# Performance work log

Hardware: AMD Instinct MI355X
Metric: run time of the kernel (lower is better)

## Reference

```python
import jax, jax.numpy as jnp
import numpy as np
from jax import lax

EPS = 1e-5
B = 512

def _conv(x, w, pad):
    # x: [B,Cin,H,W], w: [Cout,Cin,kh,kw]
    return lax.conv_general_dilated(x, w, (1, 1), [(pad, pad), (pad, pad)],
                                    dimension_numbers=('NCHW', 'OIHW', 'NCHW'))

def _bn2d(x, g, b, m, v):
    s = g * lax.rsqrt(v + EPS)
    return x * s[None, :, None, None] + (b - m * s)[None, :, None, None]

def _bn1d(x, g, b, m, v):
    s = g * lax.rsqrt(v + EPS)
    return x * s + (b - m * s)

def _pool2(x):
    return lax.reduce_window(x, -jnp.inf, lax.max, (1, 1, 2, 2), (1, 1, 2, 2), 'VALID')

def setup_inputs() -> dict:
    key = jax.random.key(0)
    ks = iter(jax.random.split(key, 64))
    rn = lambda shape, s=1.0: jax.random.normal(next(ks), shape, dtype=jnp.float32) * s
    un = lambda shape: jax.random.uniform(next(ks), shape, dtype=jnp.float32, minval=0.5, maxval=1.5)
    def bn_params(c):
        return (jnp.ones((c,), jnp.float32), jnp.zeros((c,), jnp.float32), rn((c,), 0.1), un((c,)))
    inp = {"x": rn((B, 3, 64, 64))}
    inp["w1"] = rn((32, 3, 5, 5), 0.1)
    inp["bn1_g"], inp["bn1_b"], inp["bn1_m"], inp["bn1_v"] = bn_params(32)
    inp["w2"] = rn((64, 32, 3, 3), 0.06)
    inp["bn2_g"], inp["bn2_b"], inp["bn2_m"], inp["bn2_v"] = bn_params(64)
    inp["w3"] = rn((128, 64, 3, 3), 0.04)
    inp["bn3_g"], inp["bn3_b"], inp["bn3_m"], inp["bn3_v"] = bn_params(128)
    inp["fc_w"] = rn((256, 8192), 0.01)
    inp["fc_b"] = jnp.zeros((256,), jnp.float32)
    inp["bnf_g"], inp["bnf_b"], inp["bnf_m"], inp["bnf_v"] = bn_params(256)
    inp["c_w1"] = rn((64, 256), 0.06)
    inp["c_b1"] = jnp.zeros((64,), jnp.float32)
    inp["bnc_g"], inp["bnc_b"], inp["bnc_m"], inp["bnc_v"] = bn_params(64)
    inp["c_w2"] = rn((1, 64), 0.1)
    inp["c_b2"] = jnp.zeros((1,), jnp.float32)
    inp["m_w1"] = rn((64, 256), 0.06)
    inp["m_b1"] = jnp.zeros((64,), jnp.float32)
    inp["bnm_g"], inp["bnm_b"], inp["bnm_m"], inp["bnm_v"] = bn_params(64)
    inp["m_w2"] = rn((1, 64), 0.1)
    inp["m_b2"] = jnp.zeros((1,), jnp.float32)
    return inp

def reference(x, w1, bn1_g, bn1_b, bn1_m, bn1_v,
              w2, bn2_g, bn2_b, bn2_m, bn2_v,
              w3, bn3_g, bn3_b, bn3_m, bn3_v,
              fc_w, fc_b, bnf_g, bnf_b, bnf_m, bnf_v,
              c_w1, c_b1, bnc_g, bnc_b, bnc_m, bnc_v, c_w2, c_b2,
              m_w1, m_b1, bnm_g, bnm_b, bnm_m, bnm_v, m_w2, m_b2):
    # Block 1: conv5x5(3->32) + BN + ReLU + maxpool2 -> [B,32,32,32]
    h = _pool2(jax.nn.relu(_bn2d(_conv(x, w1, 2), bn1_g, bn1_b, bn1_m, bn1_v)))
    # Block 2: conv3x3(32->64) + BN + ReLU + maxpool2 -> [B,64,16,16]
    h = _pool2(jax.nn.relu(_bn2d(_conv(h, w2, 1), bn2_g, bn2_b, bn2_m, bn2_v)))
    # Block 3: conv3x3(64->128) + BN + ReLU + maxpool2 + ToDense -> [B,128,8,8]
    h = _pool2(jax.nn.relu(_bn2d(_conv(h, w3, 1), bn3_g, bn3_b, bn3_m, bn3_v)))
    f = h.reshape(h.shape[0], -1)  # [B, 8192]
    s = jax.nn.relu(_bn1d(f @ fc_w.T + fc_b, bnf_g, bnf_b, bnf_m, bnf_v))  # [B,256]
    c = jax.nn.relu(_bn1d(s @ c_w1.T + c_b1, bnc_g, bnc_b, bnc_m, bnc_v)) @ c_w2.T + c_b2
    mo = jax.nn.relu(_bn1d(s @ m_w1.T + m_b1, bnm_g, bnm_b, bnm_m, bnm_v)) @ m_w2.T + m_b2
    return (c, mo)  # ([B,1], [B,1])
```

## Files before the change

kernel.cpp:

```cpp
#include <hip/hip_runtime.h>
#include <hip/hip_bf16.h>

#define EPS 1e-5f

typedef __attribute__((ext_vector_type(8))) short bf16x8;
typedef __attribute__((ext_vector_type(4))) float f32x4;

__device__ __forceinline__ ushort f2b(float f) {
    return __builtin_bit_cast(ushort, __float2bfloat16(f));
}
__device__ __forceinline__ bf16x8 ld_frag(const char* p) {
    return __builtin_bit_cast(bf16x8, *reinterpret_cast<const uint4*>(p));
}

__global__ __launch_bounds__(256) void k_prep(
    const float* __restrict__ w1, const float* __restrict__ w2,
    const float* __restrict__ w3,
    ushort* __restrict__ w1p, ushort* __restrict__ w2p, ushort* __restrict__ w3p)
{
    const int total = 5120 + 18432 + 73728;
    for (int i = blockIdx.x * 256 + threadIdx.x; i < total; i += gridDim.x * 256) {
        if (i < 5120) {
            const int ky = i >> 10, co = (i >> 5) & 31, k = i & 31;
            const int kx = k >> 2, ci = k & 3;
            float v = 0.f;
            if (kx < 5 && ci < 3) v = w1[((co * 3 + ci) * 5 + ky) * 5 + kx];
            w1p[i] = f2b(v);
        } else if (i < 5120 + 18432) {
            const int j = i - 5120;
            const int tap = j >> 11, co = (j >> 5) & 63, ci = j & 31;
            w2p[j] = f2b(w2[(co * 32 + ci) * 9 + tap]);
        } else {
            const int j = i - (5120 + 18432);
            const int tap = j >> 13, co = (j >> 6) & 127, ci = j & 63;
            w3p[j] = f2b(w3[(co * 64 + ci) * 9 + tap]);
        }
    }
}

__global__ __launch_bounds__(256) void k_prep_fc(
    const float* __restrict__ fcw, ushort* __restrict__ fcwp)
{
    __shared__ ushort l[128 * 66];
    const int j = blockIdx.x, t = threadIdx.x;
    const float* src = fcw + (size_t)j * 8192;
    #pragma unroll
    for (int i = 0; i < 32; ++i) {
        const int idx = i * 256 + t;
        const int c = idx >> 6, p = idx & 63;
        l[c * 66 + p] = f2b(src[idx]);
    }
    __syncthreads();
    ushort* dst = fcwp + (size_t)j * 8192;
    #pragma unroll
    for (int i = 0; i < 32; ++i) {
        const int idx = i * 256 + t;
        const int c = idx & 127, p = idx >> 7;
        dst[idx] = l[c * 66 + p];
    }
}

__global__ __launch_bounds__(256) void k_conv1(
    const float* __restrict__ x, const ushort* __restrict__ w1p,
    const float* __restrict__ bg, const float* __restrict__ bb,
    const float* __restrict__ bm, const float* __restrict__ bv,
    ushort* __restrict__ h1)
{
    __shared__ __align__(16) ushort xs[12 * 72 * 4];
    __shared__ __align__(16) ushort ws[5 * 32 * 32];
    const int bid = blockIdx.x;
    const int n = bid >> 3, q = bid & 7;
    const int t = threadIdx.x;
    const int wave = t >> 6, lane = t & 63;
    const int g = lane >> 4, l15 = lane & 15;

    for (int idx = t; idx < 864; idx += 256) {
        const int row = idx / 72, col = idx - row * 72;
        const int gr = 8 * q - 2 + row, gc = col - 2;
        ushort p0 = 0, p1 = 0, p2 = 0;
        if ((unsigned)gr < 64u && (unsigned)gc < 64u) {
            const size_t base = ((size_t)n * 3 << 12) + (gr << 6) + gc;
            p0 = f2b(x[base]); p1 = f2b(x[base + 4096]); p2 = f2b(x[base + 8192]);
        }
        ushort4 pk; pk.x = p0; pk.y = p1; pk.z = p2; pk.w = 0;
        *reinterpret_cast<ushort4*>(&xs[idx * 4]) = pk;
    }
    for (int i = t; i < 640; i += 256) {
        const int gg = i & 3, r = i >> 2;
        const int co = r & 31;
        const uint4 v = *reinterpret_cast<const uint4*>(&w1p[r * 32 + gg * 8]);
        *reinterpret_cast<uint4*>((char*)ws + r * 64 + ((gg ^ ((co >> 1) & 3)) << 4)) = v;
    }
    __syncthreads();

    f32x4 acc[8][2];
    #pragma unroll
    for (int i = 0; i < 8; ++i) { acc[i][0] = (f32x4){0,0,0,0}; acc[i][1] = (f32x4){0,0,0,0}; }

    const char* xsb = (const char*)xs;
    const char* wsb = (const char*)ws;
    #pragma unroll
    for (int ky = 0; ky < 5; ++ky) {
        bf16x8 a[8], b[2];
        #pragma unroll
        for (int mt = 0; mt < 8; ++mt) {
            const int crl = 2 * wave + (mt >> 2);
            const int ccl = (mt & 3) * 16 + l15;
            const int off = ((crl + ky) * 72 + ccl) * 8 + g * 16;
            const uint2 lo = *reinterpret_cast<const uint2*>(xsb + off);
            const uint2 hi = *reinterpret_cast<const uint2*>(xsb + off + 8);
            uint4 all; all.x = lo.x; all.y = lo.y; all.z = hi.x; all.w = hi.y;
            a[mt] = __builtin_bit_cast(bf16x8, all);
        }
        #pragma unroll
        for (int nt = 0; nt < 2; ++nt) {
            const int co = nt * 16 + l15;
            b[nt] = ld_frag(wsb + (ky * 32 + co) * 64 + ((g ^ ((co >> 1) & 3)) << 4));
        }
        #pragma unroll
        for (int mt = 0; mt < 8; ++mt)
            #pragma unroll
            for (int nt = 0; nt < 2; ++nt)
                acc[mt][nt] = __builtin_amdgcn_mfma_f32_16x16x32_bf16(a[mt], b[nt], acc[mt][nt], 0, 0, 0);
    }

    const int prow = q * 4 + wave;
    #pragma unroll
    for (int nt = 0; nt < 2; ++nt) {
        const int co = nt * 16 + l15;
        const float s = bg[co] * rsqrtf(bv[co] + EPS);
        const float bsv = bb[co] - bm[co] * s;
        #pragma unroll
        for (int mt = 0; mt < 4; ++mt) {
            #pragma unroll
            for (int j = 0; j < 2; ++j) {
                const float v0 = fmaxf(fmaf(acc[mt][nt][2 * j],     s, bsv), 0.f);
                const float v1 = fmaxf(fmaf(acc[mt][nt][2 * j + 1], s, bsv), 0.f);
                const float v2 = fmaxf(fmaf(acc[mt + 4][nt][2 * j],     s, bsv), 0.f);
                const float v3 = fmaxf(fmaf(acc[mt + 4][nt][2 * j + 1], s, bsv), 0.f);
                const int ppc = mt * 8 + g * 2 + j;
                h1[(((size_t)n * 32 + prow) * 32 + ppc) * 32 + co] =
                    f2b(fmaxf(fmaxf(v0, v1), fmaxf(v2, v3)));
            }
        }
    }
}

__global__ __launch_bounds__(256) void k_conv2(
    const ushort* __restrict__ h1, const ushort* __restrict__ w2p,
    const float* __restrict__ bg, const float* __restrict__ bb,
    const float* __restrict__ bm, const float* __restrict__ bv,
    ushort* __restrict__ h2)
{
    __shared__ __align__(16) ushort xs[10 * 34 * 32];
    __shared__ __align__(16) ushort ws[9 * 64 * 32];
    const int bid = blockIdx.x;
    const int n = bid >> 2, q = bid & 3;
    const int t = threadIdx.x;
    const int wave = t >> 6, lane = t & 63;
    const int g = lane >> 4, l15 = lane & 15;

    for (int i = t; i < 1360; i += 256) {
        const int gg = i & 3, pix = i >> 2;
        const int row = pix / 34, col = pix - row * 34;
        const int gr = 8 * q - 1 + row, gc = col - 1;
        uint4 v = {0, 0, 0, 0};
        if ((unsigned)gr < 32u && (unsigned)gc < 32u)
            v = *reinterpret_cast<const uint4*>(&h1[((((size_t)n * 32 + gr) * 32 + gc) << 5) + gg * 8]);
        *reinterpret_cast<uint4*>((char*)xs + pix * 64 + ((gg ^ ((pix >> 1) & 3)) << 4)) = v;
    }
    for (int i = t; i < 2304; i += 256) {
        const int gg = i & 3, r = i >> 2;
        const int co = r & 63;
        const uint4 v = *reinterpret_cast<const uint4*>(&w2p[r * 32 + gg * 8]);
        *reinterpret_cast<uint4*>((char*)ws + r * 64 + ((gg ^ ((co >> 1) & 3)) << 4)) = v;
    }
    __syncthreads();

    f32x4 acc[4][4];
    #pragma unroll
    for (int i = 0; i < 4; ++i)
        #pragma unroll
        for (int j = 0; j < 4; ++j) acc[i][j] = (f32x4){0,0,0,0};

    const char* xsb = (const char*)xs;
    const char* wsb = (const char*)ws;
    #pragma unroll
    for (int tap = 0; tap < 9; ++tap) {
        const int ky = tap / 3, kx = tap - 3 * ky;
        bf16x8 a[4], b[4];
        #pragma unroll
        for (int mt = 0; mt < 4; ++mt) {
            const int crl = 2 * wave + (mt >> 1);
            const int ccl = (mt & 1) * 16 + l15;
            const int pix = (crl + ky) * 34 + ccl + kx;
            a[mt] = ld_frag(xsb + pix * 64 + ((g ^ ((pix >> 1) & 3)) << 4));
        }
        #pragma unroll
        for (int nt = 0; nt < 4; ++nt) {
            const int co = nt * 16 + l15;
            b[nt] = ld_frag(wsb + (tap * 64 + co) * 64 + ((g ^ ((co >> 1) & 3)) << 4));
        }
        #pragma unroll
        for (int mt = 0; mt < 4; ++mt)
            #pragma unroll
            for (int nt = 0; nt < 4; ++nt)
                acc[mt][nt] = __builtin_amdgcn_mfma_f32_16x16x32_bf16(a[mt], b[nt], acc[mt][nt], 0, 0, 0);
    }
    __syncthreads();

    const int prow = q * 4 + wave;
    #pragma unroll
    for (int nt = 0; nt < 4; ++nt) {
        const int co = nt * 16 + l15;
        const float s = bg[co] * rsqrtf(bv[co] + EPS);
        const float bsv = bb[co] - bm[co] * s;
        #pragma unroll
        for (int mtl = 0; mtl < 2; ++mtl) {
            #pragma unroll
            for (int j = 0; j < 2; ++j) {
                const float v0 = fmaxf(fmaf(acc[mtl][nt][2 * j],     s, bsv), 0.f);
                const float v1 = fmaxf(fmaf(acc[mtl][nt][2 * j + 1], s, bsv), 0.f);
                const float v2 = fmaxf(fmaf(acc[mtl + 2][nt][2 * j],     s, bsv), 0.f);
                const float v3 = fmaxf(fmaf(acc[mtl + 2][nt][2 * j + 1], s, bsv), 0.f);
                const int ppc = mtl * 8 + g * 2 + j;
                h2[(((size_t)n * 16 + prow) * 16 + ppc) * 64 + co] =
                    f2b(fmaxf(fmaxf(v0, v1), fmaxf(v2, v3)));
            }
        }
    }
}

__global__ __launch_bounds__(256) void k_conv3(
    const ushort* __restrict__ h2, const ushort* __restrict__ w3p,
    const float* __restrict__ bg, const float* __restrict__ bb,
    const float* __restrict__ bm, const float* __restrict__ bv,
    ushort* __restrict__ h3)
{
    __shared__ __align__(16) ushort xs[18 * 18 * 32];
    __shared__ __align__(16) ushort ws[9 * 64 * 32];
    const int bid = blockIdx.x;
    const int n = bid >> 1, ch = bid & 1;
    const int t = threadIdx.x;
    const int wave = t >> 6, lane = t & 63;
    const int g = lane >> 4, l15 = lane & 15;

    f32x4 acc[4][4];
    #pragma unroll
    for (int i = 0; i < 4; ++i)
        #pragma unroll
        for (int j = 0; j < 4; ++j) acc[i][j] = (f32x4){0,0,0,0};

    const char* xsb = (const char*)xs;
    const char* wsb = (const char*)ws;

    for (int gci = 0; gci < 2; ++gci) {
        if (gci) __syncthreads();
        for (int i = t; i < 1296; i += 256) {
            const int gg = i & 3, pix = i >> 2;
            const int row = pix / 18, col = pix - row * 18;
            const int gr = row - 1, gc = col - 1;
            uint4 v = {0, 0, 0, 0};
            if ((unsigned)gr < 16u && (unsigned)gc < 16u)
                v = *reinterpret_cast<const uint4*>(
                    &h2[((((size_t)n * 16 + gr) * 16 + gc) << 6) + gci * 32 + gg * 8]);
            *reinterpret_cast<uint4*>((char*)xs + pix * 64 + ((gg ^ ((pix >> 1) & 3)) << 4)) = v;
        }
        for (int i = t; i < 2304; i += 256) {
            const int gg = i & 3, r = i >> 2;
            const int tap = r >> 6, co = r & 63;
            const uint4 v = *reinterpret_cast<const uint4*>(
                &w3p[((size_t)(tap * 128 + ch * 64 + co) << 6) + gci * 32 + gg * 8]);
            *reinterpret_cast<uint4*>((char*)ws + r * 64 + ((gg ^ ((co >> 1) & 3)) << 4)) = v;
        }
        __syncthreads();
        #pragma unroll
        for (int tap = 0; tap < 9; ++tap) {
            const int ky = tap / 3, kx = tap - 3 * ky;
            bf16x8 a[4], b[4];
            #pragma unroll
            for (int mt = 0; mt < 4; ++mt) {
                const int pr = 4 * wave + mt;
                const int pix = (pr + ky) * 18 + l15 + kx;
                a[mt] = ld_frag(xsb + pix * 64 + ((g ^ ((pix >> 1) & 3)) << 4));
            }
            #pragma unroll
            for (int nt = 0; nt < 4; ++nt) {
                const int co = nt * 16 + l15;
                b[nt] = ld_frag(wsb + (tap * 64 + co) * 64 + ((g ^ ((co >> 1) & 3)) << 4));
            }
            #pragma unroll
            for (int mt = 0; mt < 4; ++mt)
                #pragma unroll
                for (int nt = 0; nt < 4; ++nt)
                    acc[mt][nt] = __builtin_amdgcn_mfma_f32_16x16x32_bf16(a[mt], b[nt], acc[mt][nt], 0, 0, 0);
        }
    }

    #pragma unroll
    for (int nt = 0; nt < 4; ++nt) {
        const int co = ch * 64 + nt * 16 + l15;
        const float s = bg[co] * rsqrtf(bv[co] + EPS);
        const float bsv = bb[co] - bm[co] * s;
        #pragma unroll
        for (int mtl = 0; mtl < 2; ++mtl) {
            #pragma unroll
            for (int j = 0; j < 2; ++j) {
                const int mt = mtl * 2;
                const float v0 = fmaxf(fmaf(acc[mt][nt][2 * j],     s, bsv), 0.f);
                const float v1 = fmaxf(fmaf(acc[mt][nt][2 * j + 1], s, bsv), 0.f);
                const float v2 = fmaxf(fmaf(acc[mt + 1][nt][2 * j],     s, bsv), 0.f);
                const float v3 = fmaxf(fmaf(acc[mt + 1][nt][2 * j + 1], s, bsv), 0.f);
                const int ppr = 2 * wave + mtl;
                const int ppc = g * 2 + j;
                h3[(((size_t)n * 8 + ppr) * 8 + ppc) * 128 + co] =
                    f2b(fmaxf(fmaxf(v0, v1), fmaxf(v2, v3)));
            }
        }
    }
}

__global__ __launch_bounds__(256) void k_fc(
    const ushort* __restrict__ A, const ushort* __restrict__ Bw, float* __restrict__ C)
{
    __shared__ __align__(16) ushort As[64 * 32];
    __shared__ __align__(16) ushort Bs[64 * 32];
    const int bm = blockIdx.x, bn = blockIdx.y, kz = blockIdx.z;
    const int t = threadIdx.x;
    const int wave = t >> 6, lane = t & 63;
    const int g = lane >> 4, l15 = lane & 15;

    f32x4 acc[4];
    #pragma unroll
    for (int i = 0; i < 4; ++i) acc[i] = (f32x4){0,0,0,0};

    const char* asb = (const char*)As;
    const char* bsb = (const char*)Bs;
    for (int kk = 0; kk < 16; ++kk) {
        const int k0 = kz * 512 + kk * 32;
        if (kk) __syncthreads();
        {
            const int gg = t & 3, row = t >> 2;
            const uint4 va = *reinterpret_cast<const uint4*>(
                &A[(size_t)(bm * 64 + row) * 8192 + k0 + gg * 8]);
            *reinterpret_cast<uint4*>((char*)As + row * 64 + ((gg ^ ((row >> 1) & 3)) << 4)) = va;
            const uint4 vb = *reinterpret_cast<const uint4*>(
                &Bw[(size_t)(bn * 64 + row) * 8192 + k0 + gg * 8]);
            *reinterpret_cast<uint4*>((char*)Bs + row * 64 + ((gg ^ ((row >> 1) & 3)) << 4)) = vb;
        }
        __syncthreads();
        bf16x8 a[4], b;
        #pragma unroll
        for (int mt = 0; mt < 4; ++mt) {
            const int r = mt * 16 + l15;
            a[mt] = ld_frag(asb + r * 64 + ((g ^ ((r >> 1) & 3)) << 4));
        }
        {
            const int r = wave * 16 + l15;
            b = ld_frag(bsb + r * 64 + ((g ^ ((r >> 1) & 3)) << 4));
        }
        #pragma unroll
        for (int mt = 0; mt < 4; ++mt)
            acc[mt] = __builtin_amdgcn_mfma_f32_16x16x32_bf16(a[mt], b, acc[mt], 0, 0, 0);
    }

    float* Cp = C + (size_t)kz * 512 * 256;
    const int col = bn * 64 + wave * 16 + l15;
    #pragma unroll
    for (int mt = 0; mt < 4; ++mt) {
        #pragma unroll
        for (int r = 0; r < 4; ++r) {
            const int row = bm * 64 + mt * 16 + g * 4 + r;
            Cp[(size_t)row * 256 + col] = acc[mt][r];
        }
    }
}

__global__ __launch_bounds__(128) void k_heads(
    const float* __restrict__ sraw, const float* __restrict__ fcb,
    const float* __restrict__ fg, const float* __restrict__ fb,
    const float* __restrict__ fm, const float* __restrict__ fv,
    const float* __restrict__ cw1, const float* __restrict__ cb1,
    const float* __restrict__ cg, const float* __restrict__ cbb,
    const float* __restrict__ cm, const float* __restrict__ cv,
    const float* __restrict__ cw2, const float* __restrict__ cb2,
    const float* __restrict__ mw1, const float* __restrict__ mb1,
    const float* __restrict__ mg, const float* __restrict__ mbb,
    const float* __restrict__ mm, const float* __restrict__ mv,
    const float* __restrict__ mw2, const float* __restrict__ mb2,
    float* __restrict__ outp)
{
    __shared__ float sv[256];
    const int b = blockIdx.x, t = threadIdx.x;
    for (int k = t; k < 256; k += 128) {
        float val = fcb[k];
        #pragma unroll
        for (int z = 0; z < 16; ++z) val += sraw[(size_t)z * 131072 + b * 256 + k];
        const float s = fg[k] * rsqrtf(fv[k] + EPS);
        sv[k] = fmaxf(fmaf(val, s, fb[k] - fm[k] * s), 0.f);
    }
    __syncthreads();
    const int j = t & 63;
    const bool isM = (t >= 64);
    const float* w1  = isM ? mw1 : cw1;
    const float* b1  = isM ? mb1 : cb1;
    const float* g1  = isM ? mg  : cg;
    const float* bb1 = isM ? mbb : cbb;
    const float* m1  = isM ? mm  : cm;
    const float* v1  = isM ? mv  : cv;
    const float* w2  = isM ? mw2 : cw2;
    const float* b2  = isM ? mb2 : cb2;
    float d = 0.f;
    const float* wr = w1 + j * 256;
    #pragma unroll 8
    for (int k = 0; k < 256; ++k) d = fmaf(sv[k], wr[k], d);
    d += b1[j];
    const float s1 = g1[j] * rsqrtf(v1[j] + EPS);
    d = fmaxf(fmaf(d, s1, bb1[j] - m1[j] * s1), 0.f);
    float prod = d * w2[j];
    #pragma unroll
    for (int off = 32; off > 0; off >>= 1) prod += __shfl_down(prod, off);
    if (j == 0) outp[(isM ? 512 : 0) + b] = prod + b2[0];
}

extern "C" void kernel_launch(void* const* d_in, const int* in_sizes, int n_in,
                              void* d_out, int out_size, void* d_ws, size_t ws_size,
                              hipStream_t stream)
{
    const float* x    = (const float*)d_in[0];
    const float* w1   = (const float*)d_in[1];
    const float* bn1g = (const float*)d_in[2];
    const float* bn1b = (const float*)d_in[3];
    const float* bn1m = (const float*)d_in[4];
    const float* bn1v = (const float*)d_in[5];
    const float* w2   = (const float*)d_in[6];
    const float* bn2g = (const float*)d_in[7];
    const float* bn2b = (const float*)d_in[8];
    const float* bn2m = (const float*)d_in[9];
    const float* bn2v = (const float*)d_in[10];
    const float* w3   = (const float*)d_in[11];
    const float* bn3g = (const float*)d_in[12];
    const float* bn3b = (const float*)d_in[13];
    const float* bn3m = (const float*)d_in[14];
    const float* bn3v = (const float*)d_in[15];
    const float* fcw  = (const float*)d_in[16];
    const float* fcb  = (const float*)d_in[17];
    const float* bnfg = (const float*)d_in[18];
    const float* bnfb = (const float*)d_in[19];
    const float* bnfm = (const float*)d_in[20];
    const float* bnfv = (const float*)d_in[21];
    const float* cw1  = (const float*)d_in[22];
    const float* cb1  = (const float*)d_in[23];
    const float* bncg = (const float*)d_in[24];
    const float* bncb = (const float*)d_in[25];
    const float* bncm = (const float*)d_in[26];
    const float* bncv = (const float*)d_in[27];
    const float* cw2  = (const float*)d_in[28];
    const float* cb2  = (const float*)d_in[29];
    const float* mw1  = (const float*)d_in[30];
    const float* mb1  = (const float*)d_in[31];
    const float* bnmg = (const float*)d_in[32];
    const float* bnmb = (const float*)d_in[33];
    const float* bnmm = (const float*)d_in[34];
    const float* bnmv = (const float*)d_in[35];
    const float* mw2  = (const float*)d_in[36];
    const float* mb2  = (const float*)d_in[37];

    char* W = (char*)d_ws;
    ushort* h1   = (ushort*)(W);
    ushort* h2   = (ushort*)(W + 33554432);
    ushort* h3   = (ushort*)(W + 50331648);
    ushort* w1p  = (ushort*)(W + 58720256);
    ushort* w2p  = (ushort*)(W + 58730496);
    ushort* w3p  = (ushort*)(W + 58767360);
    ushort* fcwp = (ushort*)(W + 58914816);
    float*  sr   = (float*) (W + 63109120);
    float* outp = (float*)d_out;

    k_prep<<<128, 256, 0, stream>>>(w1, w2, w3, w1p, w2p, w3p);
    k_prep_fc<<<256, 256, 0, stream>>>(fcw, fcwp);
    k_conv1<<<512 * 8, 256, 0, stream>>>(x, w1p, bn1g, bn1b, bn1m, bn1v, h1);
    k_conv2<<<512 * 4, 256, 0, stream>>>(h1, w2p, bn2g, bn2b, bn2m, bn2v, h2);
    k_conv3<<<512 * 2, 256, 0, stream>>>(h2, w3p, bn3g, bn3b, bn3m, bn3v, h3);
    k_fc<<<dim3(8, 4, 16), 256, 0, stream>>>(h3, fcwp, sr);
    k_heads<<<512, 128, 0, stream>>>(sr, fcb, bnfg, bnfb, bnfm, bnfv,
                                     cw1, cb1, bncg, bncb, bncm, bncv, cw2, cb2,
                                     mw1, mb1, bnmg, bnmb, bnmm, bnmv, mw2, mb2, outp);
}
```

Measured before the change: 254.4 us.

## Pre-pad activations in global memory, merge prep kernels, and batch images per conv block

All prep work is merged into one kernel. That kernel also converts the input to a zero-padded, 4-channel bf16 layout and zeroes the halo borders of padded h1 and h2 buffers. Conv1 and conv2 then write into these padded buffers, so conv2 and conv3 can load tiles with plain vectorized copies and no bounds checks. Conv2 now loops over 4 images per block, and conv3 has each block handle 2 images with more M tiles per wave, so weights staged in shared memory are reused. The costs are an extra pass over the input, a larger workspace, fewer blocks, and higher register pressure in conv3.

```diff
diff --git a/kernel.cpp b/kernel.cpp
--- a/kernel.cpp
+++ b/kernel.cpp
@@ -13,58 +13,97 @@
     return __builtin_bit_cast(bf16x8, *reinterpret_cast<const uint4*>(p));
 }
 
-__global__ __launch_bounds__(256) void k_prep(
+__global__ __launch_bounds__(256) void k_prep_all(
     const float* __restrict__ w1, const float* __restrict__ w2,
-    const float* __restrict__ w3,
-    ushort* __restrict__ w1p, ushort* __restrict__ w2p, ushort* __restrict__ w3p)
-{
-    const int total = 5120 + 18432 + 73728;
-    for (int i = blockIdx.x * 256 + threadIdx.x; i < total; i += gridDim.x * 256) {
-        if (i < 5120) {
-            const int ky = i >> 10, co = (i >> 5) & 31, k = i & 31;
-            const int kx = k >> 2, ci = k & 3;
-            float v = 0.f;
-            if (kx < 5 && ci < 3) v = w1[((co * 3 + ci) * 5 + ky) * 5 + kx];
-            w1p[i] = f2b(v);
-        } else if (i < 5120 + 18432) {
-            const int j = i - 5120;
-            const int tap = j >> 11, co = (j >> 5) & 63, ci = j & 31;
-            w2p[j] = f2b(w2[(co * 32 + ci) * 9 + tap]);
-        } else {
-            const int j = i - (5120 + 18432);
-            const int tap = j >> 13, co = (j >> 6) & 127, ci = j & 63;
-            w3p[j] = f2b(w3[(co * 64 + ci) * 9 + tap]);
-        }
-    }
-}
-
-__global__ __launch_bounds__(256) void k_prep_fc(
-    const float* __restrict__ fcw, ushort* __restrict__ fcwp)
+    const float* __restrict__ w3, const float* __restrict__ fcw,
+    const float* __restrict__ x,
+    ushort* __restrict__ w1p, ushort* __restrict__ w2p, ushort* __restrict__ w3p,
+    ushort* __restrict__ fcwp, ushort* __restrict__ x4p,
+    ushort* __restrict__ h1p, ushort* __restrict__ h2p)
 {
     __shared__ ushort l[128 * 66];
-    const int j = blockIdx.x, t = threadIdx.x;
-    const float* src = fcw + (size_t)j * 8192;
-    #pragma unroll
-    for (int i = 0; i < 32; ++i) {
-        const int idx = i * 256 + t;
-        const int c = idx >> 6, p = idx & 63;
-        l[c * 66 + p] = f2b(src[idx]);
-    }
-    __syncthreads();
-    ushort* dst = fcwp + (size_t)j * 8192;
-    #pragma unroll
-    for (int i = 0; i < 32; ++i) {
-        const int idx = i * 256 + t;
-        const int c = idx & 127, p = idx >> 7;
-        dst[idx] = l[c * 66 + p];
+    const int bid = blockIdx.x, t = threadIdx.x;
+    if (bid < 128) {
+        const int total = 5120 + 18432 + 73728;
+        for (int i = bid * 256 + t; i < total; i += 128 * 256) {
+            if (i < 5120) {
+                const int ky = i >> 10, co = (i >> 5) & 31, k = i & 31;
+                const int kx = k >> 2, ci = k & 3;
+                float v = 0.f;
+                if (kx < 5 && ci < 3) v = w1[((co * 3 + ci) * 5 + ky) * 5 + kx];
+                w1p[i] = f2b(v);
+            } else if (i < 5120 + 18432) {
+                const int j = i - 5120;
+                const int tap = j >> 11, co = (j >> 5) & 63, ci = j & 31;
+                w2p[j] = f2b(w2[(co * 32 + ci) * 9 + tap]);
+            } else {
+                const int j = i - (5120 + 18432);
+                const int tap = j >> 13, co = (j >> 6) & 127, ci = j & 63;
+                w3p[j] = f2b(w3[(co * 64 + ci) * 9 + tap]);
+            }
+        }
+    } else if (bid < 384) {
+        const int j = bid - 128;
+        const float* src = fcw + (size_t)j * 8192;
+        #pragma unroll
+        for (int i = 0; i < 32; ++i) {
+            const int idx = i * 256 + t;
+            const int c = idx >> 6, p = idx & 63;
+            l[c * 66 + p] = f2b(src[idx]);
+        }
+        __syncthreads();
+        ushort* dst = fcwp + (size_t)j * 8192;
+        #pragma unroll
+        for (int i = 0; i < 32; ++i) {
+            const int idx = i * 256 + t;
+            const int c = idx & 127, p = idx >> 7;
+            dst[idx] = l[c * 66 + p];
+        }
+    } else if (bid < 4480) {
+        for (int p = (bid - 384) * 256 + t; p < 2506752; p += 4096 * 256) {
+            const int n = p / 4896;
+            const int rem = p - n * 4896;
+            const int row = rem / 72, col = rem - row * 72;
+            const int gr = row - 2, gc = col - 2;
+            ushort4 pk; pk.x = 0; pk.y = 0; pk.z = 0; pk.w = 0;
+            if ((unsigned)gr < 64u && (unsigned)gc < 64u) {
+                const size_t base = ((size_t)n * 3 << 12) + (gr << 6) + gc;
+                pk.x = f2b(x[base]); pk.y = f2b(x[base + 4096]); pk.z = f2b(x[base + 8192]);
+            }
+            *reinterpret_cast<ushort4*>(&x4p[(size_t)p * 4]) = pk;
+        }
+    } else if (bid < 4736) {
+        const uint4 z = {0, 0, 0, 0};
+        for (int i = (bid - 4480) * 256 + t; i < 270336; i += 256 * 256) {
+            const int img = i / 528;
+            const int rem = i - img * 528;
+            const int px = rem >> 2, gg = rem & 3;
+            int row, col;
+            if (px < 34)      { row = 0;  col = px; }
+            else if (px < 68) { row = 33; col = px - 34; }
+            else { const int q = px - 68; row = 1 + (q >> 1); col = (q & 1) ? 33 : 0; }
+            *reinterpret_cast<uint4*>(&h1p[(((size_t)img * 34 + row) * 34 + col) * 32 + gg * 8]) = z;
+        }
+    } else if (bid < 4992) {
+        const uint4 z = {0, 0, 0, 0};
+        for (int i = (bid - 4736) * 256 + t; i < 278528; i += 256 * 256) {
+            const int img = i / 544;
+            const int rem = i - img * 544;
+            const int px = rem >> 3, gg = rem & 7;
+            int row, col;
+            if (px < 18)      { row = 0;  col = px; }
+            else if (px < 36) { row = 17; col = px - 18; }
+            else { const int q = px - 36; row = 1 + (q >> 1); col = (q & 1) ? 17 : 0; }
+            *reinterpret_cast<uint4*>(&h2p[(((size_t)img * 18 + row) * 18 + col) * 64 + gg * 8]) = z;
+        }
     }
 }
 
 __global__ __launch_bounds__(256) void k_conv1(
-    const float* __restrict__ x, const ushort* __restrict__ w1p,
+    const ushort* __restrict__ x4p, const ushort* __restrict__ w1p,
     const float* __restrict__ bg, const float* __restrict__ bb,
     const float* __restrict__ bm, const float* __restrict__ bv,
-    ushort* __restrict__ h1)
+    ushort* __restrict__ h1p)
 {
     __shared__ __align__(16) ushort xs[12 * 72 * 4];
     __shared__ __align__(16) ushort ws[5 * 32 * 32];
@@ -74,16 +113,10 @@
     const int wave = t >> 6, lane = t & 63;
     const int g = lane >> 4, l15 = lane & 15;
 
-    for (int idx = t; idx < 864; idx += 256) {
-        const int row = idx / 72, col = idx - row * 72;
-        const int gr = 8 * q - 2 + row, gc = col - 2;
-        ushort p0 = 0, p1 = 0, p2 = 0;
-        if ((unsigned)gr < 64u && (unsigned)gc < 64u) {
-            const size_t base = ((size_t)n * 3 << 12) + (gr << 6) + gc;
-            p0 = f2b(x[base]); p1 = f2b(x[base + 4096]); p2 = f2b(x[base + 8192]);
-        }
-        ushort4 pk; pk.x = p0; pk.y = p1; pk.z = p2; pk.w = 0;
-        *reinterpret_cast<ushort4*>(&xs[idx * 4]) = pk;
+    {
+        const ushort* src = x4p + ((size_t)(n * 68 + 8 * q) * 72) * 4;
+        for (int i = t; i < 432; i += 256)
+            *reinterpret_cast<uint4*>(&xs[i * 8]) = *reinterpret_cast<const uint4*>(src + i * 8);
     }
     for (int i = t; i < 640; i += 256) {
         const int gg = i & 3, r = i >> 2;
@@ -139,132 +172,136 @@
                 const float v2 = fmaxf(fmaf(acc[mt + 4][nt][2 * j],     s, bsv), 0.f);
                 const float v3 = fmaxf(fmaf(acc[mt + 4][nt][2 * j + 1], s, bsv), 0.f);
                 const int ppc = mt * 8 + g * 2 + j;
-                h1[(((size_t)n * 32 + prow) * 32 + ppc) * 32 + co] =
+                h1p[(((size_t)n * 34 + prow + 1) * 34 + ppc + 1) * 32 + co] =
                     f2b(fmaxf(fmaxf(v0, v1), fmaxf(v2, v3)));
             }
         }
     }
 }
 
-__global__ __launch_bounds__(256) void k_conv2(
-    const ushort* __restrict__ h1, const ushort* __restrict__ w2p,
+__global__ __launch_bounds__(256, 2) void k_conv2(
+    const ushort* __restrict__ h1p, const ushort* __restrict__ w2p,
     const float* __restrict__ bg, const float* __restrict__ bb,
     const float* __restrict__ bm, const float* __restrict__ bv,
-    ushort* __restrict__ h2)
+    ushort* __restrict__ h2p)
 {
     __shared__ __align__(16) ushort xs[10 * 34 * 32];
     __shared__ __align__(16) ushort ws[9 * 64 * 32];
     const int bid = blockIdx.x;
-    const int n = bid >> 2, q = bid & 3;
+    const int ngrp = bid >> 2, q = bid & 3;
     const int t = threadIdx.x;
     const int wave = t >> 6, lane = t & 63;
     const int g = lane >> 4, l15 = lane & 15;
-
-    for (int i = t; i < 1360; i += 256) {
-        const int gg = i & 3, pix = i >> 2;
-        const int row = pix / 34, col = pix - row * 34;
-        const int gr = 8 * q - 1 + row, gc = col - 1;
-        uint4 v = {0, 0, 0, 0};
-        if ((unsigned)gr < 32u && (unsigned)gc < 32u)
-            v = *reinterpret_cast<const uint4*>(&h1[((((size_t)n * 32 + gr) * 32 + gc) << 5) + gg * 8]);
-        *reinterpret_cast<uint4*>((char*)xs + pix * 64 + ((gg ^ ((pix >> 1) & 3)) << 4)) = v;
-    }
+    const char* xsb = (const char*)xs;
+    const char* wsb = (const char*)ws;
+
     for (int i = t; i < 2304; i += 256) {
         const int gg = i & 3, r = i >> 2;
         const int co = r & 63;
         const uint4 v = *reinterpret_cast<const uint4*>(&w2p[r * 32 + gg * 8]);
         *reinterpret_cast<uint4*>((char*)ws + r * 64 + ((gg ^ ((co >> 1) & 3)) << 4)) = v;
     }
-    __syncthreads();
-
-    f32x4 acc[4][4];
-    #pragma unroll
-    for (int i = 0; i < 4; ++i)
-        #pragma unroll
-        for (int j = 0; j < 4; ++j) acc[i][j] = (f32x4){0,0,0,0};
-
-    const char* xsb = (const char*)xs;
-    const char* wsb = (const char*)ws;
-    #pragma unroll
-    for (int tap = 0; tap < 9; ++tap) {
-        const int ky = tap / 3, kx = tap - 3 * ky;
-        bf16x8 a[4], b[4];
-        #pragma unroll
-        for (int mt = 0; mt < 4; ++mt) {
-            const int crl = 2 * wave + (mt >> 1);
-            const int ccl = (mt & 1) * 16 + l15;
-            const int pix = (crl + ky) * 34 + ccl + kx;
-            a[mt] = ld_frag(xsb + pix * 64 + ((g ^ ((pix >> 1) & 3)) << 4));
-        }
+
+    for (int img = 0; img < 4; ++img) {
+        const int n = ngrp * 4 + img;
+        if (img) __syncthreads();
+        {
+            const ushort* src = h1p + ((size_t)(n * 34 + 8 * q) * 34) * 32;
+            for (int i = t; i < 1360; i += 256) {
+                const int gg = i & 3, pix = i >> 2;
+                const uint4 v = *reinterpret_cast<const uint4*>(src + i * 8);
+                *reinterpret_cast<uint4*>((char*)xs + pix * 64 + ((gg ^ ((pix >> 1) & 3)) << 4)) = v;
+            }
+        }
+        __syncthreads();
+
+        f32x4 acc[4][4];
+        #pragma unroll
+        for (int i = 0; i < 4; ++i)
+            #pragma unroll
+            for (int j = 0; j < 4; ++j) acc[i][j] = (f32x4){0,0,0,0};
+
+        #pragma unroll
+        for (int tap = 0; tap < 9; ++tap) {
+            const int ky = tap / 3, kx = tap - 3 * ky;
+            bf16x8 a[4], b[4];
+            #pragma unroll
+            for (int mt = 0; mt < 4; ++mt) {
+                const int crl = 2 * wave + (mt >> 1);
+                const int ccl = (mt & 1) * 16 + l15;
+                const int pix = (crl + ky) * 34 + ccl + kx;
+                a[mt] = ld_frag(xsb + pix * 64 + ((g ^ ((pix >> 1) & 3)) << 4));
+            }
+            #pragma unroll
+            for (int nt = 0; nt < 4; ++nt) {
+                const int co = nt * 16 + l15;
+                b[nt] = ld_frag(wsb + (tap * 64 + co) * 64 + ((g ^ ((co >> 1) & 3)) << 4));
+            }
+            #pragma unroll
+            for (int mt = 0; mt < 4; ++mt)
+                #pragma unroll
+                for (int nt = 0; nt < 4; ++nt)
+                    acc[mt][nt] = __builtin_amdgcn_mfma_f32_16x16x32_bf16(a[mt], b[nt], acc[mt][nt], 0, 0, 0);
+        }
+
+        const int prow = q * 4 + wave;
         #pragma unroll
         for (int nt = 0; nt < 4; ++nt) {
             const int co = nt * 16 + l15;
-            b[nt] = ld_frag(wsb + (tap * 64 + co) * 64 + ((g ^ ((co >> 1) & 3)) << 4));
-        }
-        #pragma unroll
-        for (int mt = 0; mt < 4; ++mt)
-            #pragma unroll
-            for (int nt = 0; nt < 4; ++nt)
-                acc[mt][nt] = __builtin_amdgcn_mfma_f32_16x16x32_bf16(a[mt], b[nt], acc[mt][nt], 0, 0, 0);
-    }
-    __syncthreads();
-
-    const int prow = q * 4 + wave;
-    #pragma unroll
-    for (int nt = 0; nt < 4; ++nt) {
-        const int co = nt * 16 + l15;
-        const float s = bg[co] * rsqrtf(bv[co] + EPS);
-        const float bsv = bb[co] - bm[co] * s;
-        #pragma unroll
-        for (int mtl = 0; mtl < 2; ++mtl) {
-            #pragma unroll
-            for (int j = 0; j < 2; ++j) {
-                const float v0 = fmaxf(fmaf(acc[mtl][nt][2 * j],     s, bsv), 0.f);
-                const float v1 = fmaxf(fmaf(acc[mtl][nt][2 * j + 1], s, bsv), 0.f);
-                const float v2 = fmaxf(fmaf(acc[mtl + 2][nt][2 * j],     s, bsv), 0.f);
-                const float v3 = fmaxf(fmaf(acc[mtl + 2][nt][2 * j + 1], s, bsv), 0.f);
-                const int ppc = mtl * 8 + g * 2 + j;
-                h2[(((size_t)n * 16 + prow) * 16 + ppc) * 64 + co] =
-                    f2b(fmaxf(fmaxf(v0, v1), fmaxf(v2, v3)));
-            }
-        }
-    }
-}
-
-__global__ __launch_bounds__(256) void k_conv3(
-    const ushort* __restrict__ h2, const ushort* __restrict__ w3p,
+            const float s = bg[co] * rsqrtf(bv[co] + EPS);
+            const float bsv = bb[co] - bm[co] * s;
+            #pragma unroll
+            for (int mtl = 0; mtl < 2; ++mtl) {
+                #pragma unroll
+                for (int j = 0; j < 2; ++j) {
+                    const float v0 = fmaxf(fmaf(acc[mtl][nt][2 * j],     s, bsv), 0.f);
+                    const float v1 = fmaxf(fmaf(acc[mtl][nt][2 * j + 1], s, bsv), 0.f);
+                    const float v2 = fmaxf(fmaf(acc[mtl + 2][nt][2 * j],     s, bsv), 0.f);
+                    const float v3 = fmaxf(fmaf(acc[mtl + 2][nt][2 * j + 1], s, bsv), 0.f);
+                    const int ppc = mtl * 8 + g * 2 + j;
+                    h2p[(((size_t)n * 18 + prow + 1) * 18 + ppc + 1) * 64 + co] =
+                        f2b(fmaxf(fmaxf(v0, v1), fmaxf(v2, v3)));
+                }
+            }
+        }
+    }
+}
+
+__global__ __launch_bounds__(256, 2) void k_conv3(
+    const ushort* __restrict__ h2p, const ushort* __restrict__ w3p,
     const float* __restrict__ bg, const float* __restrict__ bb,
     const float* __restrict__ bm, const float* __restrict__ bv,
     ushort* __restrict__ h3)
 {
-    __shared__ __align__(16) ushort xs[18 * 18 * 32];
+    __shared__ __align__(16) ushort xs[2 * 324 * 32];
     __shared__ __align__(16) ushort ws[9 * 64 * 32];
     const int bid = blockIdx.x;
-    const int n = bid >> 1, ch = bid & 1;
+    const int ngrp = bid >> 1, ch = bid & 1;
     const int t = threadIdx.x;
     const int wave = t >> 6, lane = t & 63;
+    const int wl = wave & 1, imgw = wave >> 1;
+    const int n = ngrp * 2 + imgw;
     const int g = lane >> 4, l15 = lane & 15;
-
-    f32x4 acc[4][4];
-    #pragma unroll
-    for (int i = 0; i < 4; ++i)
-        #pragma unroll
-        for (int j = 0; j < 4; ++j) acc[i][j] = (f32x4){0,0,0,0};
-
     const char* xsb = (const char*)xs;
     const char* wsb = (const char*)ws;
 
+    f32x4 acc[8][4];
+    #pragma unroll
+    for (int i = 0; i < 8; ++i)
+        #pragma unroll
+        for (int j = 0; j < 4; ++j) acc[i][j] = (f32x4){0,0,0,0};
+
     for (int gci = 0; gci < 2; ++gci) {
         if (gci) __syncthreads();
-        for (int i = t; i < 1296; i += 256) {
-            const int gg = i & 3, pix = i >> 2;
-            const int row = pix / 18, col = pix - row * 18;
-            const int gr = row - 1, gc = col - 1;
-            uint4 v = {0, 0, 0, 0};
-            if ((unsigned)gr < 16u && (unsigned)gc < 16u)
-                v = *reinterpret_cast<const uint4*>(
-                    &h2[((((size_t)n * 16 + gr) * 16 + gc) << 6) + gci * 32 + gg * 8]);
-            *reinterpret_cast<uint4*>((char*)xs + pix * 64 + ((gg ^ ((pix >> 1) & 3)) << 4)) = v;
+        for (int i = t; i < 2592; i += 256) {
+            const int img2 = i / 1296;
+            const int rem = i - img2 * 1296;
+            const int pix = rem >> 2, gg = rem & 3;
+            const int nsrc = ngrp * 2 + img2;
+            const uint4 v = *reinterpret_cast<const uint4*>(
+                &h2p[((size_t)nsrc * 324 + pix) * 64 + gci * 32 + gg * 8]);
+            *reinterpret_cast<uint4*>((char*)xs + img2 * 20736 + pix * 64 +
+                                      ((gg ^ ((pix >> 1) & 3)) << 4)) = v;
         }
         for (int i = t; i < 2304; i += 256) {
             const int gg = i & 3, r = i >> 2;
@@ -277,12 +314,12 @@
         #pragma unroll
         for (int tap = 0; tap < 9; ++tap) {
             const int ky = tap / 3, kx = tap - 3 * ky;
-            bf16x8 a[4], b[4];
-            #pragma unroll
-            for (int mt = 0; mt < 4; ++mt) {
-                const int pr = 4 * wave + mt;
+            bf16x8 a[8], b[4];
+            #pragma unroll
+            for (int mt = 0; mt < 8; ++mt) {
+                const int pr = 8 * wl + mt;
                 const int pix = (pr + ky) * 18 + l15 + kx;
-                a[mt] = ld_frag(xsb + pix * 64 + ((g ^ ((pix >> 1) & 3)) << 4));
+                a[mt] = ld_frag(xsb + imgw * 20736 + pix * 64 + ((g ^ ((pix >> 1) & 3)) << 4));
             }
             #pragma unroll
             for (int nt = 0; nt < 4; ++nt) {
@@ -290,7 +327,7 @@
                 b[nt] = ld_frag(wsb + (tap * 64 + co) * 64 + ((g ^ ((co >> 1) & 3)) << 4));
             }
             #pragma unroll
-            for (int mt = 0; mt < 4; ++mt)
+            for (int mt = 0; mt < 8; ++mt)
                 #pragma unroll
                 for (int nt = 0; nt < 4; ++nt)
                     acc[mt][nt] = __builtin_amdgcn_mfma_f32_16x16x32_bf16(a[mt], b[nt], acc[mt][nt], 0, 0, 0);
@@ -303,17 +340,16 @@
         const float s = bg[co] * rsqrtf(bv[co] + EPS);
         const float bsv = bb[co] - bm[co] * s;
         #pragma unroll
-        for (int mtl = 0; mtl < 2; ++mtl) {
+        for (int k = 0; k < 4; ++k) {
             #pragma unroll
             for (int j = 0; j < 2; ++j) {
-                const int mt = mtl * 2;
-                const float v0 = fmaxf(fmaf(acc[mt][nt][2 * j],     s, bsv), 0.f);
-                const float v1 = fmaxf(fmaf(acc[mt][nt][2 * j + 1], s, bsv), 0.f);
-                const float v2 = fmaxf(fmaf(acc[mt + 1][nt][2 * j],     s, bsv), 0.f);
-                const float v3 = fmaxf(fmaf(acc[mt + 1][nt][2 * j + 1], s, bsv), 0.f);
-                const int ppr = 2 * wave + mtl;
-                const int ppc = g * 2 + j;
-                h3[(((size_t)n * 8 + ppr) * 8 + ppc) * 128 + co] =
+                const float v0 = fmaxf(fmaf(acc[2 * k][nt][2 * j],     s, bsv), 0.f);
+                const float v1 = fmaxf(fmaf(acc[2 * k][nt][2 * j + 1], s, bsv), 0.f);
+                const float v2 = fmaxf(fmaf(acc[2 * k + 1][nt][2 * j],     s, bsv), 0.f);
+                const float v3 = fmaxf(fmaf(acc[2 * k + 1][nt][2 * j + 1], s, bsv), 0.f);
+                const int ppr = 4 * wl + k;
+                const int pcol = g * 2 + j;
+                h3[(((size_t)n * 8 + ppr) * 8 + pcol) * 128 + co] =
                     f2b(fmaxf(fmaxf(v0, v1), fmaxf(v2, v3)));
             }
         }
@@ -467,21 +503,22 @@
     const float* mb2  = (const float*)d_in[37];
 
     char* W = (char*)d_ws;
-    ushort* h1   = (ushort*)(W);
-    ushort* h2   = (ushort*)(W + 33554432);
-    ushort* h3   = (ushort*)(W + 50331648);
-    ushort* w1p  = (ushort*)(W + 58720256);
-    ushort* w2p  = (ushort*)(W + 58730496);
-    ushort* w3p  = (ushort*)(W + 58767360);
-    ushort* fcwp = (ushort*)(W + 58914816);
-    float*  sr   = (float*) (W + 63109120);
+    ushort* x4p  = (ushort*)(W);
+    ushort* h1p  = (ushort*)(W + 20054016);
+    ushort* h2p  = (ushort*)(W + 57933824);
+    ushort* h3   = (ushort*)(W + 79167488);
+    ushort* w1p  = (ushort*)(W + 87556096);
+    ushort* w2p  = (ushort*)(W + 87566336);
+    ushort* w3p  = (ushort*)(W + 87603200);
+    ushort* fcwp = (ushort*)(W + 87750656);
+    float*  sr   = (float*) (W + 91944960);
     float* outp = (float*)d_out;
 
-    k_prep<<<128, 256, 0, stream>>>(w1, w2, w3, w1p, w2p, w3p);
-    k_prep_fc<<<256, 256, 0, stream>>>(fcw, fcwp);
-    k_conv1<<<512 * 8, 256, 0, stream>>>(x, w1p, bn1g, bn1b, bn1m, bn1v, h1);
-    k_conv2<<<512 * 4, 256, 0, stream>>>(h1, w2p, bn2g, bn2b, bn2m, bn2v, h2);
-    k_conv3<<<512 * 2, 256, 0, stream>>>(h2, w3p, bn3g, bn3b, bn3m, bn3v, h3);
+    k_prep_all<<<4992, 256, 0, stream>>>(w1, w2, w3, fcw, x,
+                                         w1p, w2p, w3p, fcwp, x4p, h1p, h2p);
+    k_conv1<<<512 * 8, 256, 0, stream>>>(x4p, w1p, bn1g, bn1b, bn1m, bn1v, h1p);
+    k_conv2<<<128 * 4, 256, 0, stream>>>(h1p, w2p, bn2g, bn2b, bn2m, bn2v, h2p);
+    k_conv3<<<256 * 2, 256, 0, stream>>>(h2p, w3p, bn3g, bn3b, bn3m, bn3v, h3);
     k_fc<<<dim3(8, 4, 16), 256, 0, stream>>>(h3, fcwp, sr);
     k_heads<<<512, 128, 0, stream>>>(sr, fcb, bnfg, bnfb, bnfm, bnfv,
                                      cw1, cb1, bncg, bncb, bncm, bncv, cw2, cb2,
```

Measured after the change: 261.2 us. 1.03x slower.
